# Kernel optimization log

Hardware: AMD Instinct MI355X
Metric: run time of the kernel (lower is better)

## Reference

```python
import jax, jax.numpy as jnp
import numpy as np

ARCH = [128, 64, 32]
HIDDEN = 256
N_NODES = 20000
N_EDGES = 640000


def setup_inputs() -> dict:
    key = jax.random.key(0)
    ks = jax.random.split(key, 10)
    s = lambda fan_in: 1.0 / np.sqrt(fan_in)
    inp = {
        "x": jax.random.normal(ks[0], (N_NODES, ARCH[0]), dtype=jnp.float32),
        "edge_index": jax.random.randint(ks[1], (2, N_EDGES), 0, N_NODES, dtype=jnp.int64),
        # embedding: Linear(arch[0], hidden)
        "emb_W": jax.random.uniform(ks[2], (HIDDEN, ARCH[0]), jnp.float32, -s(ARCH[0]), s(ARCH[0])),
        "emb_b": jax.random.uniform(ks[3], (HIDDEN,), jnp.float32, -s(ARCH[0]), s(ARCH[0])),
        # message: Linear(hidden, hidden)
        "msg_W": jax.random.uniform(ks[4], (HIDDEN, HIDDEN), jnp.float32, -s(HIDDEN), s(HIDDEN)),
        "msg_b": jax.random.uniform(ks[5], (HIDDEN,), jnp.float32, -s(HIDDEN), s(HIDDEN)),
        # output_layers[0]: Linear(hidden, arch[0]*arch[1]) = 256 -> 8192
        "W0": jax.random.uniform(ks[6], (ARCH[0] * ARCH[1], HIDDEN), jnp.float32, -s(HIDDEN), s(HIDDEN)),
        "b0": jax.random.uniform(ks[7], (ARCH[0] * ARCH[1],), jnp.float32, -s(HIDDEN), s(HIDDEN)),
        # output_layers[1]: Linear(hidden, arch[1]*arch[2]) = 256 -> 2048
        "W1": jax.random.uniform(ks[8], (ARCH[1] * ARCH[2], HIDDEN), jnp.float32, -s(HIDDEN), s(HIDDEN)),
        "b1": jax.random.uniform(ks[9], (ARCH[1] * ARCH[2],), jnp.float32, -s(HIDDEN), s(HIDDEN)),
    }
    return inp


def reference(x, edge_index, emb_W, emb_b, msg_W, msg_b, W0, b0, W1, b1):
    # h = relu(embedding(x)): [N, hidden]
    h = jax.nn.relu(x @ emb_W.T + emb_b)
    row, col = edge_index[0], edge_index[1]
    # gather messages from source nodes, scatter-add into destinations
    agg = jnp.zeros_like(h).at[row].add(h[col])  # [N, hidden]
    h = jax.nn.relu(agg @ msg_W.T + msg_b)       # [N, hidden]
    # per-layer weight prediction: linear, reshape, mean over nodes
    w0 = (h @ W0.T + b0).mean(axis=0).reshape(ARCH[0], ARCH[1])  # [128, 64]
    w1 = (h @ W1.T + b1).mean(axis=0).reshape(ARCH[1], ARCH[2])  # [64, 32]
    return (w0, w1)
```

## Files before the change

### kernel.cpp

```cpp
#include <hip/hip_runtime.h>
#include <hip/hip_bf16.h>

#define N_NODES 20000
#define N_EDGES 640000
#define HID 256
#define INDIM 128

#define WS_H_OFF    0u
#define WS_AGG_OFF  5120000u
#define WS_XBF_OFF  15360000u
#define WS_EW_OFF   20480000u
#define WS_MW_OFF   20545536u
#define WS_CS_OFF   20676608u
#define WS_DEG_OFF  20677632u
#define WS_ROW_OFF  20757632u
#define WS_SRC_OFF  20837760u
#define WS_NEEDED   23397760u

#define X_ELEMS  (N_NODES * INDIM)
#define EW_ELEMS (HID * INDIM)
#define MW_ELEMS (HID * HID)
#define CONV_BLOCKS ((X_ELEMS + EW_ELEMS + MW_ELEMS) / 8 / 256)
#define ZERO_BYTES  (1024 + 80000)
#define ZERO_F4     (ZERO_BYTES / 16)
#define ZERO_BLOCKS ((ZERO_F4 + 255) / 256)

#define EMB_BLOCKS  ((N_NODES + 63) / 64)
#define CNT_BLOCKS  (N_EDGES / 256)

typedef __attribute__((ext_vector_type(8))) short bf16x8;
typedef __attribute__((ext_vector_type(4))) float f32x4;
typedef __attribute__((ext_vector_type(2))) float f32x2;

__device__ inline unsigned short f2bf(float v) {
    union { float f; unsigned int u; } c; c.f = v;
    unsigned int lsb = (c.u >> 16) & 1u;
    c.u += 0x7fffu + lsb;
    return (unsigned short)(c.u >> 16);
}
__device__ inline float bf2f(unsigned short u) {
    union { float f; unsigned int u; } c; c.u = ((unsigned int)u) << 16;
    return c.f;
}

__device__ inline unsigned char f2fp8(float v) {
    union { float f; unsigned int u; } c; c.f = v;
    if (v == 0.f) return 0;
    int e = (int)((c.u >> 23) & 0xff) - 127;
    if (e >= -6) {
        unsigned int mant = c.u & 0x7fffffu;
        unsigned int base = ((unsigned int)(e + 7) << 3) | (mant >> 20);
        unsigned int rem  = mant & 0xfffffu;
        base += (rem > 0x80000u) || (rem == 0x80000u && (base & 1u));
        return (unsigned char)base;
    } else {
        return (unsigned char)__builtin_rintf(v * 512.0f);
    }
}

__global__ __launch_bounds__(256) void k_convert(const float* __restrict__ x,
                                                 const float* __restrict__ eW,
                                                 const float* __restrict__ mW,
                                                 unsigned short* __restrict__ xbf,
                                                 unsigned short* __restrict__ eWbf,
                                                 unsigned short* __restrict__ mWbf,
                                                 float4* __restrict__ zbase)
{
    if (blockIdx.x >= CONV_BLOCKS) {
        const int zi = (blockIdx.x - CONV_BLOCKS) * 256 + threadIdx.x;
        if (zi < ZERO_F4) zbase[zi] = make_float4(0.f, 0.f, 0.f, 0.f);
        return;
    }
    const int t = blockIdx.x * 256 + threadIdx.x;
    const int i8 = t * 8;
    const float* src;
    unsigned short* dst;
    int off;
    if (i8 < X_ELEMS)                 { src = x;  dst = xbf;  off = i8; }
    else if (i8 < X_ELEMS + EW_ELEMS) { src = eW; dst = eWbf; off = i8 - X_ELEMS; }
    else                              { src = mW; dst = mWbf; off = i8 - X_ELEMS - EW_ELEMS; }

    float4 a = *(const float4*)(src + off);
    float4 b = *(const float4*)(src + off + 4);
    unsigned short o[8] = { f2bf(a.x), f2bf(a.y), f2bf(a.z), f2bf(a.w),
                            f2bf(b.x), f2bf(b.y), f2bf(b.z), f2bf(b.w) };
    *(bf16x8*)(dst + off) = *(bf16x8*)o;
}

__global__ __launch_bounds__(256) void k_embed_count(const unsigned short* __restrict__ xbf,
                                                     const unsigned short* __restrict__ Wbf,
                                                     const float* __restrict__ b,
                                                     unsigned char* __restrict__ h8,
                                                     const int* __restrict__ ei,
                                                     int* __restrict__ deg)
{
    if (blockIdx.x >= EMB_BLOCKS) {
        const int e = (blockIdx.x - EMB_BLOCKS) * 256 + threadIdx.x;
        if (e < N_EDGES) atomicAdd(&deg[ei[e]], 1);
        return;
    }

    const int tid  = threadIdx.x;
    const int wave = tid >> 6;
    const int lane = tid & 63;
    const int lr   = lane & 15;
    const int lq   = lane >> 4;
    const int n0   = blockIdx.x * 64;
    const int colbase = wave * 64;

    f32x4 acc[4][4] = {};

#pragma unroll
    for (int kk = 0; kk < INDIM; kk += 32) {
        bf16x8 a[4], bb[4];
#pragma unroll
        for (int g = 0; g < 4; ++g)
            a[g] = *(const bf16x8*)(xbf + (size_t)(n0 + g * 16 + lr) * INDIM + kk + lq * 8);
#pragma unroll
        for (int c = 0; c < 4; ++c)
            bb[c] = *(const bf16x8*)(Wbf + (size_t)(colbase + c * 16 + lr) * INDIM + kk + lq * 8);
#pragma unroll
        for (int g = 0; g < 4; ++g)
#pragma unroll
            for (int c = 0; c < 4; ++c)
                acc[g][c] = __builtin_amdgcn_mfma_f32_16x16x32_bf16(a[g], bb[c], acc[g][c], 0, 0, 0);
    }

#pragma unroll
    for (int c = 0; c < 4; ++c) {
        const int j = colbase + c * 16 + lr;
        const float bias = b[j];
#pragma unroll
        for (int g = 0; g < 4; ++g) {
            const int nbase = n0 + g * 16 + lq * 4;
#pragma unroll
            for (int r = 0; r < 4; ++r) {
                const int n = nbase + r;
                if (n < N_NODES) {
                    float v = acc[g][c][r] + bias;
                    v = v > 0.f ? v : 0.f;
                    h8[(size_t)n * HID + j] = f2fp8(v);
                }
            }
        }
    }
}

__global__ __launch_bounds__(1024) void k_scan(const int* __restrict__ deg,
                                               int* __restrict__ rowstart)
{
    __shared__ int sums[1024];
    const int t = threadIdx.x;
    const int per = 20;
    const int base = t * per;

    int local[per];
    int s = 0;
#pragma unroll
    for (int i = 0; i < per; ++i) {
        int idx = base + i;
        int v = (idx < N_NODES) ? deg[idx] : 0;
        local[i] = s;
        s += v;
    }
    sums[t] = s;
    __syncthreads();

    for (int off = 1; off < 1024; off <<= 1) {
        int v = 0;
        if (t >= off) v = sums[t - off];
        __syncthreads();
        if (t >= off) sums[t] += v;
        __syncthreads();
    }

    const int pre = (t == 0) ? 0 : sums[t - 1];
#pragma unroll
    for (int i = 0; i < per; ++i) {
        int idx = base + i;
        if (idx < N_NODES) rowstart[idx] = pre + local[i];
    }
    if (t == 1023) rowstart[N_NODES] = sums[1023];
}

__global__ __launch_bounds__(256) void k_fill(const int* __restrict__ ei,
                                              const int* __restrict__ rowstart,
                                              int* __restrict__ deg,
                                              int* __restrict__ srcs)
{
    const int e = blockIdx.x * 256 + threadIdx.x;
    if (e >= N_EDGES) return;
    const int dst = ei[e];
    const int src = ei[N_EDGES + e];
    const int pos = rowstart[dst] + atomicSub(&deg[dst], 1) - 1;
    srcs[pos] = src;
}

__global__ __launch_bounds__(256) void k_gather(const int* __restrict__ rowstart,
                                                const int* __restrict__ srcs,
                                                const unsigned char* __restrict__ h8,
                                                unsigned short* __restrict__ aggbf)
{
    const int wid  = (blockIdx.x * 256 + threadIdx.x) >> 6;
    const int lane = threadIdx.x & 63;
    if (wid >= N_NODES) return;

    const int s0 = rowstart[wid];
    const int s1 = rowstart[wid + 1];

    float4 acc = make_float4(0.f, 0.f, 0.f, 0.f);
    const unsigned int* h32 = (const unsigned int*)h8;

    int e = s0;
    for (; e + 7 < s1; e += 8) {
        int s[8];
#pragma unroll
        for (int k = 0; k < 8; ++k) s[k] = srcs[e + k];
        unsigned int v[8];
#pragma unroll
        for (int k = 0; k < 8; ++k) v[k] = h32[(size_t)s[k] * 64 + lane];
#pragma unroll
        for (int k = 0; k < 8; ++k) {
            f32x2 lo = __builtin_amdgcn_cvt_pk_f32_fp8(v[k], false);
            f32x2 hi = __builtin_amdgcn_cvt_pk_f32_fp8(v[k], true);
            acc.x += lo[0]; acc.y += lo[1]; acc.z += hi[0]; acc.w += hi[1];
        }
    }
    for (; e < s1; ++e) {
        unsigned int va = h32[(size_t)srcs[e] * 64 + lane];
        f32x2 lo = __builtin_amdgcn_cvt_pk_f32_fp8(va, false);
        f32x2 hi = __builtin_amdgcn_cvt_pk_f32_fp8(va, true);
        acc.x += lo[0]; acc.y += lo[1]; acc.z += hi[0]; acc.w += hi[1];
    }

    ushort4 o;
    o.x = f2bf(acc.x); o.y = f2bf(acc.y); o.z = f2bf(acc.z); o.w = f2bf(acc.w);
    ((ushort4*)aggbf)[(size_t)wid * 64 + lane] = o;
}

__global__ __launch_bounds__(256) void k_msg_mfma(const unsigned short* __restrict__ aggbf,
                                                  const unsigned short* __restrict__ Wbf,
                                                  const float* __restrict__ b,
                                                  float* __restrict__ colsum)
{
    const int tid  = threadIdx.x;
    const int wave = tid >> 6;
    const int lane = tid & 63;
    const int lr   = lane & 15;
    const int lq   = lane >> 4;
    const int n0   = blockIdx.x * 64;
    const int colbase = wave * 64;

    f32x4 acc[4][4] = {};

#pragma unroll
    for (int kk = 0; kk < HID; kk += 32) {
        bf16x8 a[4], bb[4];
#pragma unroll
        for (int g = 0; g < 4; ++g)
            a[g] = *(const bf16x8*)(aggbf + (size_t)(n0 + g * 16 + lr) * HID + kk + lq * 8);
#pragma unroll
        for (int c = 0; c < 4; ++c)
            bb[c] = *(const bf16x8*)(Wbf + (size_t)(colbase + c * 16 + lr) * HID + kk + lq * 8);
#pragma unroll
        for (int g = 0; g < 4; ++g)
#pragma unroll
            for (int c = 0; c < 4; ++c)
                acc[g][c] = __builtin_amdgcn_mfma_f32_16x16x32_bf16(a[g], bb[c], acc[g][c], 0, 0, 0);
    }

#pragma unroll
    for (int c = 0; c < 4; ++c) {
        const int j = colbase + c * 16 + lr;
        const float bias = b[j];
        float part = 0.f;
#pragma unroll
        for (int g = 0; g < 4; ++g) {
            if (n0 + g * 16 < N_NODES) {
#pragma unroll
                for (int r = 0; r < 4; ++r) {
                    float v = acc[g][c][r] + bias;
                    part += v > 0.f ? v : 0.f;
                }
            }
        }
        part += __shfl_xor(part, 16);
        part += __shfl_xor(part, 32);
        if (lane < 16) unsafeAtomicAdd(&colsum[j], part);
    }
}

__global__ __launch_bounds__(256) void k_out(const float* __restrict__ colsum,
                                             const float* __restrict__ W0,
                                             const float* __restrict__ b0,
                                             const float* __restrict__ W1,
                                             const float* __restrict__ b1,
                                             float* __restrict__ out)
{
    __shared__ float hm[HID];
    const int tid = threadIdx.x;
    hm[tid] = colsum[tid] * (1.0f / (float)N_NODES);
    __syncthreads();

    const int o = blockIdx.x * 256 + tid;
    const float* Wr;
    float bias;
    if (o < 8192) { Wr = W0 + (size_t)o * HID; bias = b0[o]; }
    else          { int o1 = o - 8192; Wr = W1 + (size_t)o1 * HID; bias = b1[o1]; }

    float s = bias;
    const float4* w4 = (const float4*)Wr;
    const float4* h4 = (const float4*)hm;
#pragma unroll 8
    for (int q = 0; q < 64; ++q) {
        float4 wv = w4[q];
        float4 hv = h4[q];
        s += wv.x * hv.x + wv.y * hv.y + wv.z * hv.z + wv.w * hv.w;
    }
    out[o] = s;
}

extern "C" void kernel_launch(void* const* d_in, const int* in_sizes, int n_in,
                              void* d_out, int out_size, void* d_ws, size_t ws_size,
                              hipStream_t stream)
{
    const float* x     = (const float*)d_in[0];
    const int*   ei    = (const int*)d_in[1];
    const float* emb_W = (const float*)d_in[2];
    const float* emb_b = (const float*)d_in[3];
    const float* msg_W = (const float*)d_in[4];
    const float* msg_b = (const float*)d_in[5];
    const float* W0    = (const float*)d_in[6];
    const float* b0    = (const float*)d_in[7];
    const float* W1    = (const float*)d_in[8];
    const float* b1    = (const float*)d_in[9];
    float* out = (float*)d_out;

    char* ws = (char*)d_ws;
    unsigned char*  h8    = (unsigned char*)(ws + WS_H_OFF);
    unsigned short* aggbf = (unsigned short*)(ws + WS_AGG_OFF);
    unsigned short* xbf   = (unsigned short*)(ws + WS_XBF_OFF);
    unsigned short* eWbf  = (unsigned short*)(ws + WS_EW_OFF);
    unsigned short* mWbf  = (unsigned short*)(ws + WS_MW_OFF);
    float* colsum = (float*)(ws + WS_CS_OFF);
    int* deg      = (int*)(ws + WS_DEG_OFF);
    int* rowstart = (int*)(ws + WS_ROW_OFF);
    int* srcs     = (int*)(ws + WS_SRC_OFF);

    k_convert<<<CONV_BLOCKS + ZERO_BLOCKS, 256, 0, stream>>>(
        x, emb_W, msg_W, xbf, eWbf, mWbf, (float4*)(ws + WS_CS_OFF));

    k_embed_count<<<EMB_BLOCKS + CNT_BLOCKS, 256, 0, stream>>>(
        xbf, eWbf, emb_b, h8, ei, deg);

    k_scan<<<1, 1024, 0, stream>>>(deg, rowstart);
    k_fill<<<CNT_BLOCKS, 256, 0, stream>>>(ei, rowstart, deg, srcs);

    k_gather<<<(N_NODES * 64 + 255) / 256, 256, 0, stream>>>(rowstart, srcs, h8, aggbf);

    k_msg_mfma<<<EMB_BLOCKS, 256, 0, stream>>>(aggbf, mWbf, msg_b, colsum);

    k_out<<<(8192 + 2048) / 256, 256, 0, stream>>>(colsum, W0, b0, W1, b1, out);
}
```

Baseline: 143.1 us.

## Convert x to bf16 inside embed kernel and widen gather loads per wave

The embedding kernel now reads fp32 x directly and packs it to bf16 in registers, so the separate conversion pass over x and its workspace buffer are no longer needed. The gather kernel is restructured: each wave loads a chunk of up to 64 neighbor indices at once and broadcasts them with shuffles. Each quarter-wave then reads a full 16-byte slice of a different source row, so four edges are in flight per load instruction, and the partial sums are combined with cross-lane xor shuffles. The aim is fewer memory passes and more memory-level parallelism in the gather. In exchange it adds shuffle overhead, and the bf16 rounding for x now uses round-half-up rather than round-to-nearest-even.

```diff
diff --git a/kernel.cpp b/kernel.cpp
--- a/kernel.cpp
+++ b/kernel.cpp
@@ -8,19 +8,17 @@
 
 #define WS_H_OFF    0u
 #define WS_AGG_OFF  5120000u
-#define WS_XBF_OFF  15360000u
-#define WS_EW_OFF   20480000u
-#define WS_MW_OFF   20545536u
-#define WS_CS_OFF   20676608u
-#define WS_DEG_OFF  20677632u
-#define WS_ROW_OFF  20757632u
-#define WS_SRC_OFF  20837760u
-#define WS_NEEDED   23397760u
-
-#define X_ELEMS  (N_NODES * INDIM)
+#define WS_EW_OFF   15360000u
+#define WS_MW_OFF   15425536u
+#define WS_CS_OFF   15556608u
+#define WS_DEG_OFF  15557632u
+#define WS_ROW_OFF  15637632u
+#define WS_SRC_OFF  15717760u
+#define WS_NEEDED   18277760u
+
 #define EW_ELEMS (HID * INDIM)
 #define MW_ELEMS (HID * HID)
-#define CONV_BLOCKS ((X_ELEMS + EW_ELEMS + MW_ELEMS) / 8 / 256)
+#define CONV_BLOCKS ((EW_ELEMS + MW_ELEMS) / 8 / 256)
 #define ZERO_BYTES  (1024 + 80000)
 #define ZERO_F4     (ZERO_BYTES / 16)
 #define ZERO_BLOCKS ((ZERO_F4 + 255) / 256)
@@ -37,10 +35,6 @@
     unsigned int lsb = (c.u >> 16) & 1u;
     c.u += 0x7fffu + lsb;
     return (unsigned short)(c.u >> 16);
-}
-__device__ inline float bf2f(unsigned short u) {
-    union { float f; unsigned int u; } c; c.u = ((unsigned int)u) << 16;
-    return c.f;
 }
 
 __device__ inline unsigned char f2fp8(float v) {
@@ -58,10 +52,8 @@
     }
 }
 
-__global__ __launch_bounds__(256) void k_convert(const float* __restrict__ x,
-                                                 const float* __restrict__ eW,
+__global__ __launch_bounds__(256) void k_convert(const float* __restrict__ eW,
                                                  const float* __restrict__ mW,
-                                                 unsigned short* __restrict__ xbf,
                                                  unsigned short* __restrict__ eWbf,
                                                  unsigned short* __restrict__ mWbf,
                                                  float4* __restrict__ zbase)
@@ -76,9 +68,8 @@
     const float* src;
     unsigned short* dst;
     int off;
-    if (i8 < X_ELEMS)                 { src = x;  dst = xbf;  off = i8; }
-    else if (i8 < X_ELEMS + EW_ELEMS) { src = eW; dst = eWbf; off = i8 - X_ELEMS; }
-    else                              { src = mW; dst = mWbf; off = i8 - X_ELEMS - EW_ELEMS; }
+    if (i8 < EW_ELEMS) { src = eW; dst = eWbf; off = i8; }
+    else               { src = mW; dst = mWbf; off = i8 - EW_ELEMS; }
 
     float4 a = *(const float4*)(src + off);
     float4 b = *(const float4*)(src + off + 4);
@@ -87,7 +78,7 @@
     *(bf16x8*)(dst + off) = *(bf16x8*)o;
 }
 
-__global__ __launch_bounds__(256) void k_embed_count(const unsigned short* __restrict__ xbf,
+__global__ __launch_bounds__(256) void k_embed_count(const float* __restrict__ x,
                                                      const unsigned short* __restrict__ Wbf,
                                                      const float* __restrict__ b,
                                                      unsigned char* __restrict__ h8,
@@ -114,8 +105,17 @@
     for (int kk = 0; kk < INDIM; kk += 32) {
         bf16x8 a[4], bb[4];
 #pragma unroll
-        for (int g = 0; g < 4; ++g)
-            a[g] = *(const bf16x8*)(xbf + (size_t)(n0 + g * 16 + lr) * INDIM + kk + lq * 8);
+        for (int g = 0; g < 4; ++g) {
+            const float* xr = x + (size_t)(n0 + g * 16 + lr) * INDIM + kk + lq * 8;
+            uint4 p0 = *(const uint4*)xr;
+            uint4 p1 = *(const uint4*)(xr + 4);
+            union { unsigned u[4]; bf16x8 v; } pk;
+            pk.u[0] = ((p0.x + 0x8000u) >> 16) | ((p0.y + 0x8000u) & 0xFFFF0000u);
+            pk.u[1] = ((p0.z + 0x8000u) >> 16) | ((p0.w + 0x8000u) & 0xFFFF0000u);
+            pk.u[2] = ((p1.x + 0x8000u) >> 16) | ((p1.y + 0x8000u) & 0xFFFF0000u);
+            pk.u[3] = ((p1.z + 0x8000u) >> 16) | ((p1.w + 0x8000u) & 0xFFFF0000u);
+            a[g] = pk.v;
+        }
 #pragma unroll
         for (int c = 0; c < 4; ++c)
             bb[c] = *(const bf16x8*)(Wbf + (size_t)(colbase + c * 16 + lr) * INDIM + kk + lq * 8);
@@ -207,35 +207,77 @@
 
     const int s0 = rowstart[wid];
     const int s1 = rowstart[wid + 1];
-
-    float4 acc = make_float4(0.f, 0.f, 0.f, 0.f);
-    const unsigned int* h32 = (const unsigned int*)h8;
-
-    int e = s0;
-    for (; e + 7 < s1; e += 8) {
-        int s[8];
-#pragma unroll
-        for (int k = 0; k < 8; ++k) s[k] = srcs[e + k];
-        unsigned int v[8];
-#pragma unroll
-        for (int k = 0; k < 8; ++k) v[k] = h32[(size_t)s[k] * 64 + lane];
-#pragma unroll
-        for (int k = 0; k < 8; ++k) {
-            f32x2 lo = __builtin_amdgcn_cvt_pk_f32_fp8(v[k], false);
-            f32x2 hi = __builtin_amdgcn_cvt_pk_f32_fp8(v[k], true);
-            acc.x += lo[0]; acc.y += lo[1]; acc.z += hi[0]; acc.w += hi[1];
-        }
-    }
-    for (; e < s1; ++e) {
-        unsigned int va = h32[(size_t)srcs[e] * 64 + lane];
-        f32x2 lo = __builtin_amdgcn_cvt_pk_f32_fp8(va, false);
-        f32x2 hi = __builtin_amdgcn_cvt_pk_f32_fp8(va, true);
-        acc.x += lo[0]; acc.y += lo[1]; acc.z += hi[0]; acc.w += hi[1];
-    }
-
-    ushort4 o;
-    o.x = f2bf(acc.x); o.y = f2bf(acc.y); o.z = f2bf(acc.z); o.w = f2bf(acc.w);
-    ((ushort4*)aggbf)[(size_t)wid * 64 + lane] = o;
+    const int qslot = lane >> 4;
+    const int coff  = lane & 15;
+
+    float4 acc[4] = { {0,0,0,0}, {0,0,0,0}, {0,0,0,0}, {0,0,0,0} };
+
+#define DEC(V)                                                            \
+    {   f32x2 t_;                                                         \
+        t_ = __builtin_amdgcn_cvt_pk_f32_fp8((V).x, false);               \
+        acc[0].x += t_[0]; acc[0].y += t_[1];                             \
+        t_ = __builtin_amdgcn_cvt_pk_f32_fp8((V).x, true);                \
+        acc[0].z += t_[0]; acc[0].w += t_[1];                             \
+        t_ = __builtin_amdgcn_cvt_pk_f32_fp8((V).y, false);               \
+        acc[1].x += t_[0]; acc[1].y += t_[1];                             \
+        t_ = __builtin_amdgcn_cvt_pk_f32_fp8((V).y, true);                \
+        acc[1].z += t_[0]; acc[1].w += t_[1];                             \
+        t_ = __builtin_amdgcn_cvt_pk_f32_fp8((V).z, false);               \
+        acc[2].x += t_[0]; acc[2].y += t_[1];                             \
+        t_ = __builtin_amdgcn_cvt_pk_f32_fp8((V).z, true);                \
+        acc[2].z += t_[0]; acc[2].w += t_[1];                             \
+        t_ = __builtin_amdgcn_cvt_pk_f32_fp8((V).w, false);               \
+        acc[3].x += t_[0]; acc[3].y += t_[1];                             \
+        t_ = __builtin_amdgcn_cvt_pk_f32_fp8((V).w, true);                \
+        acc[3].z += t_[0]; acc[3].w += t_[1];  }
+
+    for (int base = s0; base < s1; base += 64) {
+        const int rem = s1 - base;
+        const int cnt = rem < 64 ? rem : 64;
+        const int idx = (lane < rem) ? srcs[base + lane] : 0;
+        int k = 0;
+        for (; k + 8 <= cnt; k += 8) {
+            const int sA = __shfl(idx, k + qslot);
+            const int sB = __shfl(idx, k + 4 + qslot);
+            uint4 vA = *((const uint4*)(h8 + (size_t)sA * 256) + coff);
+            uint4 vB = *((const uint4*)(h8 + (size_t)sB * 256) + coff);
+            DEC(vA);
+            DEC(vB);
+        }
+        for (; k < cnt; k += 4) {
+            const int sA = __shfl(idx, k + qslot);
+            uint4 v = *((const uint4*)(h8 + (size_t)sA * 256) + coff);
+            if (k + qslot >= cnt) { v.x = 0; v.y = 0; v.z = 0; v.w = 0; }
+            DEC(v);
+        }
+    }
+#undef DEC
+
+#pragma unroll
+    for (int j = 0; j < 4; ++j) {
+        acc[j].x += __shfl_xor(acc[j].x, 16);
+        acc[j].y += __shfl_xor(acc[j].y, 16);
+        acc[j].z += __shfl_xor(acc[j].z, 16);
+        acc[j].w += __shfl_xor(acc[j].w, 16);
+        acc[j].x += __shfl_xor(acc[j].x, 32);
+        acc[j].y += __shfl_xor(acc[j].y, 32);
+        acc[j].z += __shfl_xor(acc[j].z, 32);
+        acc[j].w += __shfl_xor(acc[j].w, 32);
+    }
+
+    if (qslot == 0) {
+        unsigned short o[16];
+#pragma unroll
+        for (int j = 0; j < 4; ++j) {
+            o[j * 4 + 0] = f2bf(acc[j].x);
+            o[j * 4 + 1] = f2bf(acc[j].y);
+            o[j * 4 + 2] = f2bf(acc[j].z);
+            o[j * 4 + 3] = f2bf(acc[j].w);
+        }
+        unsigned short* dst = aggbf + (size_t)wid * HID + coff * 16;
+        *(bf16x8*)dst       = *(bf16x8*)o;
+        *(bf16x8*)(dst + 8) = *(bf16x8*)(o + 8);
+    }
 }
 
 __global__ __launch_bounds__(256) void k_msg_mfma(const unsigned short* __restrict__ aggbf,
@@ -339,7 +381,6 @@
     char* ws = (char*)d_ws;
     unsigned char*  h8    = (unsigned char*)(ws + WS_H_OFF);
     unsigned short* aggbf = (unsigned short*)(ws + WS_AGG_OFF);
-    unsigned short* xbf   = (unsigned short*)(ws + WS_XBF_OFF);
     unsigned short* eWbf  = (unsigned short*)(ws + WS_EW_OFF);
     unsigned short* mWbf  = (unsigned short*)(ws + WS_MW_OFF);
     float* colsum = (float*)(ws + WS_CS_OFF);
@@ -348,10 +389,10 @@
     int* srcs     = (int*)(ws + WS_SRC_OFF);
 
     k_convert<<<CONV_BLOCKS + ZERO_BLOCKS, 256, 0, stream>>>(
-        x, emb_W, msg_W, xbf, eWbf, mWbf, (float4*)(ws + WS_CS_OFF));
+        emb_W, msg_W, eWbf, mWbf, (float4*)(ws + WS_CS_OFF));
 
     k_embed_count<<<EMB_BLOCKS + CNT_BLOCKS, 256, 0, stream>>>(
-        xbf, eWbf, emb_b, h8, ei, deg);
+        x, eWbf, emb_b, h8, ei, deg);
 
     k_scan<<<1, 1024, 0, stream>>>(deg, rowstart);
     k_fill<<<CNT_BLOCKS, 256, 0, stream>>>(ei, rowstart, deg, srcs);
```

New measurement: 139.6 us, median of 2. 1.03x faster.
